# Optimization experiments

Hardware: AMD Instinct MI355X
Metric: run time of the kernel (lower is better)

The kernel has to match this reference:

```python
import jax, jax.numpy as jnp
import numpy as np

D = 1024      # hidden_dim
E = 8         # num_experts
F = 512       # expert_dim


def setup_inputs() -> dict:
    key = jax.random.key(0)
    ks = jax.random.split(key, 7)
    B, N = 4, 4096
    s1 = 1.0 / np.sqrt(D)
    s2 = 1.0 / np.sqrt(F)
    return {
        "x": jax.random.normal(ks[0], (B, N, D), dtype=jnp.float32),
        "W1": jax.random.uniform(ks[1], (E, D, F), jnp.float32, -s1, s1),  # per-expert first linear
        "b1": jax.random.uniform(ks[2], (E, F), jnp.float32, -s1, s1),
        "W2": jax.random.uniform(ks[3], (E, F, D), jnp.float32, -s2, s2),  # per-expert second linear
        "b2": jax.random.uniform(ks[4], (E, D), jnp.float32, -s2, s2),
        "Wr": jax.random.uniform(ks[5], (D, E), jnp.float32, -s1, s1),    # router
        "br": jax.random.uniform(ks[6], (E,), jnp.float32, -s1, s1),
    }


def reference(x, W1, b1, W2, b2, Wr, br):
    # Router: softmax over experts per token. [B,N,E]
    router_weights = jax.nn.softmax(x @ Wr + br, axis=-1)
    # All experts on all tokens (dense soft-MoE), batched as grouped GEMMs.
    h = jax.nn.gelu(jnp.einsum('bnd,edf->bnef', x, W1) + b1, approximate=False)  # [B,N,E,F]
    y = jnp.einsum('bnef,efd->bned', h, W2) + b2[None, None]                      # [B,N,E,D]
    # Softmax-weighted combine over experts.
    return jnp.einsum('bned,bne->bnd', y, router_weights)
```

## Files before the change

### kernel.cpp

```cpp
#include <hip/hip_runtime.h>
#include <hip/hip_bf16.h>
#include <math.h>

#define MTOK 16384
#define DDIM 1024
#define EEXP 8
#define FDIM 512
#define EFK  4096

typedef __attribute__((ext_vector_type(8))) short short8;
typedef __attribute__((ext_vector_type(4))) float floatx4;

__device__ __forceinline__ void gld_lds16(const void* g, void* l) {
  __builtin_amdgcn_global_load_lds((const __attribute__((address_space(1))) void*)g,
                                   (__attribute__((address_space(3))) void*)l, 16, 0, 0);
}

__device__ __forceinline__ float gelu_fast(float v) {
  const float z  = v * 0.70710678118654752f;
  const float az = fabsf(z);
  const float t  = __builtin_amdgcn_rcpf(1.f + 0.3275911f * az);
  const float poly = t * (0.254829592f +
                     t * (-0.284496736f +
                     t * (1.421413741f +
                     t * (-1.453152027f +
                     t * 1.061405429f))));
  const float ex = __expf(-az * az);
  float erfv = 1.f - poly * ex;
  erfv = copysignf(erfv, z);
  return 0.5f * v * (1.f + erfv);
}

__global__ __launch_bounds__(256) void transpose_cast_kernel(
    const float* __restrict__ in, __hip_bfloat16* __restrict__ out, int R, int C) {
  __shared__ float tile[32][33];
  const float* inb = in + (size_t)blockIdx.z * R * C;
  __hip_bfloat16* outb = out + (size_t)blockIdx.z * R * C;
  const int c0 = blockIdx.x * 32, r0 = blockIdx.y * 32;
  const int tx = threadIdx.x & 31, ty = threadIdx.x >> 5;
#pragma unroll
  for (int i = 0; i < 4; ++i)
    tile[ty + i * 8][tx] = inb[(size_t)(r0 + ty + i * 8) * C + (c0 + tx)];
  __syncthreads();
#pragma unroll
  for (int i = 0; i < 4; ++i)
    outb[(size_t)(c0 + ty + i * 8) * R + (r0 + tx)] = __float2bfloat16(tile[tx][ty + i * 8]);
}

__global__ __launch_bounds__(256) void router_cast_kernel(
    const float* __restrict__ x, const float* __restrict__ Wr, const float* __restrict__ br,
    __hip_bfloat16* __restrict__ xbf, float* __restrict__ r) {
  const int wave = (blockIdx.x * 256 + threadIdx.x) >> 6;
  const int lane = threadIdx.x & 63;
  const float* xr = x + (size_t)wave * DDIM;
  float acc[EEXP];
#pragma unroll
  for (int e = 0; e < EEXP; ++e) acc[e] = 0.f;
#pragma unroll
  for (int i = 0; i < DDIM / 64; ++i) {
    const int d = i * 64 + lane;
    const float xv = xr[d];
    xbf[(size_t)wave * DDIM + d] = __float2bfloat16(xv);
    const float4* w4 = (const float4*)(Wr + (size_t)d * EEXP);
    const float4 w0 = w4[0], w1 = w4[1];
    acc[0] += xv * w0.x; acc[1] += xv * w0.y; acc[2] += xv * w0.z; acc[3] += xv * w0.w;
    acc[4] += xv * w1.x; acc[5] += xv * w1.y; acc[6] += xv * w1.z; acc[7] += xv * w1.w;
  }
#pragma unroll
  for (int off = 32; off; off >>= 1) {
#pragma unroll
    for (int e = 0; e < EEXP; ++e) acc[e] += __shfl_xor(acc[e], off, 64);
  }
  float mx = -1e30f;
#pragma unroll
  for (int e = 0; e < EEXP; ++e) { acc[e] += br[e]; mx = fmaxf(mx, acc[e]); }
  float s = 0.f;
#pragma unroll
  for (int e = 0; e < EEXP; ++e) { acc[e] = expf(acc[e] - mx); s += acc[e]; }
  const float inv = 1.f / s;
  if (lane < EEXP) r[(size_t)wave * EEXP + lane] = acc[lane] * inv;
}

#define BUFSZ 65536
#define AOFF  0
#define BOFF  32768

#define STAGE_A(Q1, QM, K0)                                                        \
  do {                                                                             \
    _Pragma("unroll") for (int r_ = 0; r_ < 2; ++r_) {                             \
      gld_lds16(gA + (size_t)(r_ * 128 + (QM) * 64 + wid * 8 + l3) * LDA_ +        \
                    (K0) + ((l7 ^ l3) * 8),                                        \
                ldsb + (Q1) * BUFSZ + AOFF + (QM) * 16384 +                        \
                    (r_ * 64 + wid * 8) * 128);                                    \
    }                                                                              \
  } while (0)

#define STAGE_B(Q1, QN, K0)                                                        \
  do {                                                                             \
    _Pragma("unroll") for (int r_ = 0; r_ < 2; ++r_) {                             \
      const int lin_ = r_ * 64 + wid * 8 + l3;                                     \
      gld_lds16(gB + (size_t)((lin_ >> 5) * 64 + (QN) * 32 + (lin_ & 31)) * LDB_ + \
                    (K0) + ((l7 ^ l3) * 8),                                        \
                ldsb + (Q1) * BUFSZ + BOFF + (QN) * 16384 +                        \
                    (r_ * 64 + wid * 8) * 128);                                    \
    }                                                                              \
  } while (0)

#define STAGE_ALL(Q1, K0)                                                          \
  do { STAGE_A(Q1, 0, K0); STAGE_B(Q1, 0, K0); STAGE_B(Q1, 1, K0);                 \
       STAGE_A(Q1, 1, K0); } while (0)

#define READS_A(P, QM)                                                             \
  _Pragma("unroll") for (int i_ = 0; i_ < 4; ++i_)                                 \
    _Pragma("unroll") for (int k_ = 0; k_ < 2; ++k_)                               \
      af[QM][i_][k_] = *(const short8*)(ldsb + (P) * BUFSZ + AOFF +                \
          (QM) * 16384 + (wr * 64 + i_ * 16 + lanem) * 128 +                       \
          (((k_ * 4 + laneq) ^ swz) * 16));

#define READS_B(P)                                                                 \
  _Pragma("unroll") for (int n_ = 0; n_ < 4; ++n_)                                 \
    _Pragma("unroll") for (int k_ = 0; k_ < 2; ++k_)                               \
      bf[n_][k_] = *(const short8*)(ldsb + (P) * BUFSZ + BOFF +                    \
          (n_ >> 1) * 16384 + (wc * 32 + (n_ & 1) * 16 + lanem) * 128 +            \
          (((k_ * 4 + laneq) ^ swz) * 16));

#define MFMA_Q(QM, QN)                                                             \
  _Pragma("unroll") for (int k_ = 0; k_ < 2; ++k_)                                 \
    _Pragma("unroll") for (int i_ = 0; i_ < 4; ++i_)                               \
      _Pragma("unroll") for (int j_ = 0; j_ < 2; ++j_)                             \
        acc[(QM) * 4 + i_][(QN) * 2 + j_] =                                        \
            __builtin_amdgcn_mfma_f32_16x16x32_bf16(                               \
                af[QM][i_][k_], bf[(QN) * 2 + j_][k_],                             \
                acc[(QM) * 4 + i_][(QN) * 2 + j_], 0, 0, 0);

#define LGKM(N)                                                                    \
  asm volatile("s_waitcnt lgkmcnt(" #N ")" ::: "memory");                          \
  __builtin_amdgcn_sched_barrier(0)

#define GEMM_CORE(NT)                                                              \
  STAGE_ALL(0, 0);                                                                 \
  asm volatile("s_waitcnt vmcnt(0)\n\ts_barrier" ::: "memory");                    \
  for (int kt = 0; kt < (NT); ++kt) {                                              \
    const int p_ = kt & 1;                                                         \
    if (kt + 1 < (NT)) STAGE_ALL(p_ ^ 1, (kt + 1) * 64);                           \
    READS_A(p_, 0);                                                                \
    READS_B(p_);                                                                   \
    __builtin_amdgcn_sched_barrier(0);                                             \
    READS_A(p_, 1);                                                                \
    __builtin_amdgcn_sched_barrier(0);                                             \
    LGKM(12);                                                                      \
    __builtin_amdgcn_s_setprio(1);                                                 \
    MFMA_Q(0, 0);                                                                  \
    __builtin_amdgcn_s_setprio(0);                                                 \
    LGKM(8);                                                                       \
    __builtin_amdgcn_s_setprio(1);                                                 \
    MFMA_Q(0, 1);                                                                  \
    __builtin_amdgcn_s_setprio(0);                                                 \
    LGKM(0);                                                                       \
    __builtin_amdgcn_s_setprio(1);                                                 \
    MFMA_Q(1, 1);                                                                  \
    MFMA_Q(1, 0);                                                                  \
    __builtin_amdgcn_s_setprio(0);                                                 \
    asm volatile("s_waitcnt vmcnt(0)\n\ts_barrier" ::: "memory");                  \
  }

__global__ __launch_bounds__(512, 2) void gemm_h_kernel(
    const __hip_bfloat16* __restrict__ A, const __hip_bfloat16* __restrict__ W1t,
    const float* __restrict__ b1, const float* __restrict__ r,
    __hip_bfloat16* __restrict__ Hs) {
  const int bid = blockIdx.x;
  const int strip = bid & 63, fb = (bid >> 6) & 1, e = bid >> 7;
  const int T0 = strip * 256, F0 = fb * 256;

  __shared__ char ldsb[2 * BUFSZ];

  const int tid = threadIdx.x, lane = tid & 63, wid = tid >> 6;
  const int wr = wid >> 2, wc = wid & 3;
  const int lanem = lane & 15, laneq = lane >> 4;
  const int l3 = lane >> 3, l7 = lane & 7;
  const int swz = lanem & 7;
  const int LDA_ = DDIM, LDB_ = DDIM;

  const __hip_bfloat16* gA = W1t + (size_t)e * FDIM * DDIM + (size_t)F0 * DDIM;
  const __hip_bfloat16* gB = A + (size_t)T0 * DDIM;

  floatx4 acc[8][4];
#pragma unroll
  for (int i = 0; i < 8; ++i)
#pragma unroll
    for (int j = 0; j < 4; ++j) acc[i][j] = (floatx4){0.f, 0.f, 0.f, 0.f};
  short8 af[2][4][2], bf[4][2];

  GEMM_CORE(DDIM / 64);

#pragma unroll
  for (int nj = 0; nj < 4; ++nj) {
    const int tok = T0 + wc * 64 + nj * 16 + lanem;
    const float rv = r[(size_t)tok * EEXP + e];
#pragma unroll
    for (int mi = 0; mi < 8; ++mi) {
      const int f = F0 + wr * 128 + mi * 16 + laneq * 4;
      const float4 b4 = *(const float4*)(b1 + e * FDIM + f);
      union { ushort4 u; __hip_bfloat16 h[4]; } pk;
      pk.h[0] = __float2bfloat16(gelu_fast(acc[mi][nj][0] + b4.x) * rv);
      pk.h[1] = __float2bfloat16(gelu_fast(acc[mi][nj][1] + b4.y) * rv);
      pk.h[2] = __float2bfloat16(gelu_fast(acc[mi][nj][2] + b4.z) * rv);
      pk.h[3] = __float2bfloat16(gelu_fast(acc[mi][nj][3] + b4.w) * rv);
      *(ushort4*)(Hs + (size_t)tok * EFK + e * FDIM + f) = pk.u;
    }
  }
}

__global__ __launch_bounds__(512, 2) void gemm_out_kernel(
    const __hip_bfloat16* __restrict__ Hs, const __hip_bfloat16* __restrict__ W2t,
    const float* __restrict__ b2, const float* __restrict__ r,
    float* __restrict__ out) {
  const int bid = blockIdx.x;
  const int strip = (bid >> 5) * 8 + (bid & 7);
  const int dq = (bid >> 3) & 3;
  const int T0 = strip * 256, D0 = dq * 256;

  __shared__ char ldsb[2 * BUFSZ];

  const int tid = threadIdx.x, lane = tid & 63, wid = tid >> 6;
  const int wr = wid >> 2, wc = wid & 3;
  const int lanem = lane & 15, laneq = lane >> 4;
  const int l3 = lane >> 3, l7 = lane & 7;
  const int swz = lanem & 7;
  const int LDA_ = EFK, LDB_ = EFK;

  const __hip_bfloat16* gA = W2t + (size_t)D0 * EFK;
  const __hip_bfloat16* gB = Hs + (size_t)T0 * EFK;

  floatx4 acc[8][4];
#pragma unroll
  for (int i = 0; i < 8; ++i)
#pragma unroll
    for (int j = 0; j < 4; ++j) acc[i][j] = (floatx4){0.f, 0.f, 0.f, 0.f};
  short8 af[2][4][2], bf[4][2];

  GEMM_CORE(EFK / 64);

#pragma unroll
  for (int mi = 0; mi < 8; ++mi) {
    const int d0 = D0 + wr * 128 + mi * 16 + laneq * 4;
    float4 b2v[EEXP];
#pragma unroll
    for (int e = 0; e < EEXP; ++e) b2v[e] = *(const float4*)(b2 + e * DDIM + d0);
#pragma unroll
    for (int nj = 0; nj < 4; ++nj) {
      const int tok = T0 + wc * 64 + nj * 16 + lanem;
      const float4* r4 = (const float4*)(r + (size_t)tok * EEXP);
      const float4 r0 = r4[0], r1 = r4[1];
      const float rv[EEXP] = {r0.x, r0.y, r0.z, r0.w, r1.x, r1.y, r1.z, r1.w};
      float bx = 0.f, by = 0.f, bz = 0.f, bw = 0.f;
#pragma unroll
      for (int e = 0; e < EEXP; ++e) {
        bx += rv[e] * b2v[e].x; by += rv[e] * b2v[e].y;
        bz += rv[e] * b2v[e].z; bw += rv[e] * b2v[e].w;
      }
      float4 o;
      o.x = acc[mi][nj][0] + bx; o.y = acc[mi][nj][1] + by;
      o.z = acc[mi][nj][2] + bz; o.w = acc[mi][nj][3] + bw;
      *(float4*)(out + (size_t)tok * DDIM + d0) = o;
    }
  }
}

extern "C" void kernel_launch(void* const* d_in, const int* in_sizes, int n_in,
                              void* d_out, int out_size, void* d_ws, size_t ws_size,
                              hipStream_t stream) {
  const float* x  = (const float*)d_in[0];
  const float* W1 = (const float*)d_in[1];
  const float* b1 = (const float*)d_in[2];
  const float* W2 = (const float*)d_in[3];
  const float* b2 = (const float*)d_in[4];
  const float* Wr = (const float*)d_in[5];
  const float* br = (const float*)d_in[6];
  float* out = (float*)d_out;

  char* ws = (char*)d_ws;
  __hip_bfloat16* xbf = (__hip_bfloat16*)(ws);
  __hip_bfloat16* W1t = (__hip_bfloat16*)(ws + (32u << 20));
  __hip_bfloat16* W2t = (__hip_bfloat16*)(ws + (40u << 20));
  float*          r   = (float*)(ws + (48u << 20));
  __hip_bfloat16* Hs  = (__hip_bfloat16*)(ws + (48u << 20) + (1u << 19));

  transpose_cast_kernel<<<dim3(FDIM / 32, DDIM / 32, EEXP), 256, 0, stream>>>(W1, W1t, DDIM, FDIM);
  transpose_cast_kernel<<<dim3(DDIM / 32, EFK / 32, 1), 256, 0, stream>>>(W2, W2t, EFK, DDIM);
  router_cast_kernel<<<MTOK / 4, 256, 0, stream>>>(x, Wr, br, xbf, r);
  gemm_h_kernel<<<dim3((MTOK / 256) * (FDIM / 256) * EEXP), 512, 0, stream>>>(xbf, W1t, b1, r, Hs);
  gemm_out_kernel<<<dim3((MTOK / 256) * (DDIM / 256)), 512, 0, stream>>>(Hs, W2t, b2, r, out);
}
```

Baseline: 470.1 us.

## Interleave quadrant-granular global->LDS staging with MFMA phases in GEMM core

Restructures the double-buffered GEMM main loop into four phases. Each phase reads one A or B quadrant fragment from LDS, issues the global->LDS load for a matching quadrant of a future K-tile, and runs one quarter of the MFMAs. Prefetch now runs up to two tiles ahead with partial vmcnt waits instead of draining all loads each iteration, and the A fragment register array is halved to cut VGPR pressure. The cost is many more s_barrier syncs per iteration and tighter correctness dependencies on buffer reuse timing.

```diff
diff --git a/kernel.cpp b/kernel.cpp
--- a/kernel.cpp
+++ b/kernel.cpp
@@ -106,62 +106,76 @@
     }                                                                              \
   } while (0)
 
-#define STAGE_ALL(Q1, K0)                                                          \
-  do { STAGE_A(Q1, 0, K0); STAGE_B(Q1, 0, K0); STAGE_B(Q1, 1, K0);                 \
-       STAGE_A(Q1, 1, K0); } while (0)
-
-#define READS_A(P, QM)                                                             \
+#define READS_AF(P, QM)                                                            \
   _Pragma("unroll") for (int i_ = 0; i_ < 4; ++i_)                                 \
     _Pragma("unroll") for (int k_ = 0; k_ < 2; ++k_)                               \
-      af[QM][i_][k_] = *(const short8*)(ldsb + (P) * BUFSZ + AOFF +                \
+      af[i_][k_] = *(const short8*)(ldsb + (P) * BUFSZ + AOFF +                    \
           (QM) * 16384 + (wr * 64 + i_ * 16 + lanem) * 128 +                       \
           (((k_ * 4 + laneq) ^ swz) * 16));
 
-#define READS_B(P)                                                                 \
-  _Pragma("unroll") for (int n_ = 0; n_ < 4; ++n_)                                 \
+#define READS_BH(P, QN)                                                            \
+  _Pragma("unroll") for (int j_ = 0; j_ < 2; ++j_)                                 \
     _Pragma("unroll") for (int k_ = 0; k_ < 2; ++k_)                               \
-      bf[n_][k_] = *(const short8*)(ldsb + (P) * BUFSZ + BOFF +                    \
-          (n_ >> 1) * 16384 + (wc * 32 + (n_ & 1) * 16 + lanem) * 128 +            \
+      bf[(QN) * 2 + j_][k_] = *(const short8*)(ldsb + (P) * BUFSZ + BOFF +         \
+          (QN) * 16384 + (wc * 32 + j_ * 16 + lanem) * 128 +                       \
           (((k_ * 4 + laneq) ^ swz) * 16));
 
 #define MFMA_Q(QM, QN)                                                             \
+  __builtin_amdgcn_s_setprio(1);                                                   \
   _Pragma("unroll") for (int k_ = 0; k_ < 2; ++k_)                                 \
     _Pragma("unroll") for (int i_ = 0; i_ < 4; ++i_)                               \
       _Pragma("unroll") for (int j_ = 0; j_ < 2; ++j_)                             \
         acc[(QM) * 4 + i_][(QN) * 2 + j_] =                                        \
             __builtin_amdgcn_mfma_f32_16x16x32_bf16(                               \
-                af[QM][i_][k_], bf[(QN) * 2 + j_][k_],                             \
-                acc[(QM) * 4 + i_][(QN) * 2 + j_], 0, 0, 0);
-
-#define LGKM(N)                                                                    \
-  asm volatile("s_waitcnt lgkmcnt(" #N ")" ::: "memory");                          \
+                af[i_][k_], bf[(QN) * 2 + j_][k_],                                 \
+                acc[(QM) * 4 + i_][(QN) * 2 + j_], 0, 0, 0);                       \
+  __builtin_amdgcn_s_setprio(0);
+
+#define LGKM0                                                                      \
+  asm volatile("s_waitcnt lgkmcnt(0)" ::: "memory");                               \
   __builtin_amdgcn_sched_barrier(0)
 
 #define GEMM_CORE(NT)                                                              \
-  STAGE_ALL(0, 0);                                                                 \
-  asm volatile("s_waitcnt vmcnt(0)\n\ts_barrier" ::: "memory");                    \
+  STAGE_A(0, 0, 0); STAGE_B(0, 0, 0); STAGE_B(0, 1, 0); STAGE_A(0, 1, 0);          \
+  STAGE_A(1, 0, 64); STAGE_B(1, 0, 64); STAGE_B(1, 1, 64);                         \
+  asm volatile("s_waitcnt vmcnt(6)\n\ts_barrier" ::: "memory");                    \
   for (int kt = 0; kt < (NT); ++kt) {                                              \
-    const int p_ = kt & 1;                                                         \
-    if (kt + 1 < (NT)) STAGE_ALL(p_ ^ 1, (kt + 1) * 64);                           \
-    READS_A(p_, 0);                                                                \
-    READS_B(p_);                                                                   \
+    const int p_ = kt & 1, q_ = p_ ^ 1;                                            \
+                                                       \
+    READS_AF(p_, 0);                                                               \
+    READS_BH(p_, 0);                                                               \
+    if (kt + 1 < (NT)) STAGE_A(q_, 1, (kt + 1) * 64);                              \
+    asm volatile("s_waitcnt lgkmcnt(8)" ::: "memory");                             \
     __builtin_amdgcn_sched_barrier(0);                                             \
-    READS_A(p_, 1);                                                                \
-    __builtin_amdgcn_sched_barrier(0);                                             \
-    LGKM(12);                                                                      \
-    __builtin_amdgcn_s_setprio(1);                                                 \
+    __builtin_amdgcn_s_barrier();                                                  \
+    LGKM0;                                                                         \
     MFMA_Q(0, 0);                                                                  \
-    __builtin_amdgcn_s_setprio(0);                                                 \
-    LGKM(8);                                                                       \
-    __builtin_amdgcn_s_setprio(1);                                                 \
+    __builtin_amdgcn_s_barrier();                                                  \
+                                                       \
+    READS_BH(p_, 1);                                                               \
+    if (kt + 2 < (NT)) STAGE_A(p_, 0, (kt + 2) * 64);                              \
+    __builtin_amdgcn_s_barrier();                                                  \
+    LGKM0;                                                                         \
     MFMA_Q(0, 1);                                                                  \
-    __builtin_amdgcn_s_setprio(0);                                                 \
-    LGKM(0);                                                                       \
-    __builtin_amdgcn_s_setprio(1);                                                 \
+    __builtin_amdgcn_s_barrier();                                                  \
+                                                       \
+    READS_AF(p_, 1);                                                               \
+    if (kt + 2 < (NT)) STAGE_B(p_, 1, (kt + 2) * 64);                              \
+    __builtin_amdgcn_s_barrier();                                                  \
+    LGKM0;                                                                         \
     MFMA_Q(1, 1);                                                                  \
+    __builtin_amdgcn_s_barrier();                                                  \
+                                            \
+    if (kt + 2 < (NT)) {                                                           \
+      STAGE_B(p_, 0, (kt + 2) * 64);                                               \
+      asm volatile("s_waitcnt vmcnt(6)\n\ts_barrier" ::: "memory");                \
+    } else if (kt + 1 < (NT)) {                                                    \
+      asm volatile("s_waitcnt vmcnt(0)\n\ts_barrier" ::: "memory");                \
+    } else {                                                                       \
+      __builtin_amdgcn_s_barrier();                                                \
+    }                                                                              \
     MFMA_Q(1, 0);                                                                  \
-    __builtin_amdgcn_s_setprio(0);                                                 \
-    asm volatile("s_waitcnt vmcnt(0)\n\ts_barrier" ::: "memory");                  \
+    __builtin_amdgcn_s_barrier();                                                  \
   }
 
 __global__ __launch_bounds__(512, 2) void gemm_h_kernel(
@@ -189,7 +203,7 @@
   for (int i = 0; i < 8; ++i)
 #pragma unroll
     for (int j = 0; j < 4; ++j) acc[i][j] = (floatx4){0.f, 0.f, 0.f, 0.f};
-  short8 af[2][4][2], bf[4][2];
+  short8 af[4][2], bf[4][2];
 
   GEMM_CORE(DDIM / 64);
 
@@ -237,7 +251,7 @@
   for (int i = 0; i < 8; ++i)
 #pragma unroll
     for (int j = 0; j < 4; ++j) acc[i][j] = (floatx4){0.f, 0.f, 0.f, 0.f};
-  short8 af[2][4][2], bf[4][2];
+  short8 af[4][2], bf[4][2];
 
   GEMM_CORE(EFK / 64);
 
```

New measurement: 478.6 us. Within noise of the previous version (+1.8%).

## Pre-pack weights into MFMA fragment layout and load A directly to registers

Applied to the files above, without the earlier changes.

Replaces the weight transpose-cast kernels with kernels that write W1/W2 as bf16 already laid out in MFMA A-fragment order. The GEMM kernels then load the weight operand straight from global memory into registers, prefetched one k-step ahead, instead of staging it through LDS. This halves LDS use and removes the LDS reads for A. The cost is more global loads in flight and more registers per thread. The pipeline also changes from fine-grained lgkmcnt waits to a vmcnt-based wait that keeps some loads outstanding.

```diff
diff --git a/kernel.cpp b/kernel.cpp
--- a/kernel.cpp
+++ b/kernel.cpp
@@ -31,20 +31,33 @@
   return 0.5f * v * (1.f + erfv);
 }
 
-__global__ __launch_bounds__(256) void transpose_cast_kernel(
-    const float* __restrict__ in, __hip_bfloat16* __restrict__ out, int R, int C) {
-  __shared__ float tile[32][33];
-  const float* inb = in + (size_t)blockIdx.z * R * C;
-  __hip_bfloat16* outb = out + (size_t)blockIdx.z * R * C;
-  const int c0 = blockIdx.x * 32, r0 = blockIdx.y * 32;
-  const int tx = threadIdx.x & 31, ty = threadIdx.x >> 5;
-#pragma unroll
-  for (int i = 0; i < 4; ++i)
-    tile[ty + i * 8][tx] = inb[(size_t)(r0 + ty + i * 8) * C + (c0 + tx)];
-  __syncthreads();
-#pragma unroll
-  for (int i = 0; i < 4; ++i)
-    outb[(size_t)(c0 + ty + i * 8) * R + (r0 + tx)] = __float2bfloat16(tile[tx][ty + i * 8]);
+
+__global__ __launch_bounds__(256) void frag_cast_w2(
+    const float* __restrict__ W2, __hip_bfloat16* __restrict__ W2f) {
+  const int gid  = blockIdx.x * 4 + (threadIdx.x >> 6);
+  const int lane = threadIdx.x & 63;
+  const int kb = gid >> 6, mf = gid & 63;
+  const int d  = mf * 16 + (lane & 15);
+  const int k0 = kb * 32 + (lane >> 4) * 8;
+  union { short8 v; __hip_bfloat16 h[8]; } pk;
+#pragma unroll
+  for (int i = 0; i < 8; ++i)
+    pk.h[i] = __float2bfloat16(W2[(size_t)(k0 + i) * DDIM + d]);
+  *(short8*)((char*)W2f + (size_t)gid * 1024 + lane * 16) = pk.v;
+}
+
+__global__ __launch_bounds__(256) void frag_cast_w1(
+    const float* __restrict__ W1, __hip_bfloat16* __restrict__ W1f) {
+  const int gid  = blockIdx.x * 4 + (threadIdx.x >> 6);
+  const int lane = threadIdx.x & 63;
+  const int e = gid >> 10, kb = (gid >> 5) & 31, mf = gid & 31;
+  const int f  = mf * 16 + (lane & 15);
+  const int d0 = kb * 32 + (lane >> 4) * 8;
+  union { short8 v; __hip_bfloat16 h[8]; } pk;
+#pragma unroll
+  for (int i = 0; i < 8; ++i)
+    pk.h[i] = __float2bfloat16(W1[((size_t)e * DDIM + d0 + i) * FDIM + f]);
+  *(short8*)((char*)W1f + (size_t)gid * 1024 + lane * 16) = pk.v;
 }
 
 __global__ __launch_bounds__(256) void router_cast_kernel(
@@ -81,115 +94,84 @@
   if (lane < EEXP) r[(size_t)wave * EEXP + lane] = acc[lane] * inv;
 }
 
-#define BUFSZ 65536
-#define AOFF  0
-#define BOFF  32768
-
-#define STAGE_A(Q1, QM, K0)                                                        \
-  do {                                                                             \
-    _Pragma("unroll") for (int r_ = 0; r_ < 2; ++r_) {                             \
-      gld_lds16(gA + (size_t)(r_ * 128 + (QM) * 64 + wid * 8 + l3) * LDA_ +        \
-                    (K0) + ((l7 ^ l3) * 8),                                        \
-                ldsb + (Q1) * BUFSZ + AOFF + (QM) * 16384 +                        \
-                    (r_ * 64 + wid * 8) * 128);                                    \
-    }                                                                              \
-  } while (0)
-
-#define STAGE_B(Q1, QN, K0)                                                        \
+#define BUF_B 32768
+
+#define STAGE_BQ(Q1, QN, K0)                                                       \
   do {                                                                             \
     _Pragma("unroll") for (int r_ = 0; r_ < 2; ++r_) {                             \
       const int lin_ = r_ * 64 + wid * 8 + l3;                                     \
       gld_lds16(gB + (size_t)((lin_ >> 5) * 64 + (QN) * 32 + (lin_ & 31)) * LDB_ + \
                     (K0) + ((l7 ^ l3) * 8),                                        \
-                ldsb + (Q1) * BUFSZ + BOFF + (QN) * 16384 +                        \
+                ldsb + (Q1) * BUF_B + (QN) * 16384 +                               \
                     (r_ * 64 + wid * 8) * 128);                                    \
     }                                                                              \
   } while (0)
 
-#define STAGE_ALL(Q1, K0)                                                          \
-  do { STAGE_A(Q1, 0, K0); STAGE_B(Q1, 0, K0); STAGE_B(Q1, 1, K0);                 \
-       STAGE_A(Q1, 1, K0); } while (0)
-
-#define READS_A(P, QM)                                                             \
-  _Pragma("unroll") for (int i_ = 0; i_ < 4; ++i_)                                 \
-    _Pragma("unroll") for (int k_ = 0; k_ < 2; ++k_)                               \
-      af[QM][i_][k_] = *(const short8*)(ldsb + (P) * BUFSZ + AOFF +                \
-          (QM) * 16384 + (wr * 64 + i_ * 16 + lanem) * 128 +                       \
-          (((k_ * 4 + laneq) ^ swz) * 16));
-
 #define READS_B(P)                                                                 \
   _Pragma("unroll") for (int n_ = 0; n_ < 4; ++n_)                                 \
     _Pragma("unroll") for (int k_ = 0; k_ < 2; ++k_)                               \
-      bf[n_][k_] = *(const short8*)(ldsb + (P) * BUFSZ + BOFF +                    \
+      bf[n_][k_] = *(const short8*)(ldsb + (P) * BUF_B +                           \
           (n_ >> 1) * 16384 + (wc * 32 + (n_ & 1) * 16 + lanem) * 128 +            \
           (((k_ * 4 + laneq) ^ swz) * 16));
 
-#define MFMA_Q(QM, QN)                                                             \
-  _Pragma("unroll") for (int k_ = 0; k_ < 2; ++k_)                                 \
-    _Pragma("unroll") for (int i_ = 0; i_ < 4; ++i_)                               \
-      _Pragma("unroll") for (int j_ = 0; j_ < 2; ++j_)                             \
-        acc[(QM) * 4 + i_][(QN) * 2 + j_] =                                        \
-            __builtin_amdgcn_mfma_f32_16x16x32_bf16(                               \
-                af[QM][i_][k_], bf[(QN) * 2 + j_][k_],                             \
-                acc[(QM) * 4 + i_][(QN) * 2 + j_], 0, 0, 0);
-
-#define LGKM(N)                                                                    \
-  asm volatile("s_waitcnt lgkmcnt(" #N ")" ::: "memory");                          \
-  __builtin_amdgcn_sched_barrier(0)
+#define LOAD_A8(DST, KB)                                                           \
+  _Pragma("unroll") for (int mf_ = 0; mf_ < 8; ++mf_)                              \
+    DST[mf_] = *(const short8*)(gAf + (size_t)(KB) * AKBSTRIDE + mf_ * 1024);
+
+#define MFMA32(AFR, KK)                                                            \
+  __builtin_amdgcn_s_setprio(1);                                                   \
+  _Pragma("unroll") for (int m_ = 0; m_ < 8; ++m_)                                 \
+    _Pragma("unroll") for (int n_ = 0; n_ < 4; ++n_)                               \
+      acc[m_][n_] = __builtin_amdgcn_mfma_f32_16x16x32_bf16(                       \
+          AFR[m_], bf[n_][KK], acc[m_][n_], 0, 0, 0);                              \
+  __builtin_amdgcn_s_setprio(0);
 
 #define GEMM_CORE(NT)                                                              \
-  STAGE_ALL(0, 0);                                                                 \
-  asm volatile("s_waitcnt vmcnt(0)\n\ts_barrier" ::: "memory");                    \
+                              \
+  STAGE_BQ(0, 0, 0); STAGE_BQ(0, 1, 0);                                            \
+  __builtin_amdgcn_sched_barrier(0);                                               \
+  LOAD_A8(afk0, 0); LOAD_A8(afk1, 1);                                              \
   for (int kt = 0; kt < (NT); ++kt) {                                              \
-    const int p_ = kt & 1;                                                         \
-    if (kt + 1 < (NT)) STAGE_ALL(p_ ^ 1, (kt + 1) * 64);                           \
-    READS_A(p_, 0);                                                                \
+    const int p_ = kt & 1, q_ = p_ ^ 1;                                            \
+    asm volatile("s_waitcnt vmcnt(16)\n\ts_barrier" ::: "memory");                 \
+    if (kt + 1 < (NT)) { STAGE_BQ(q_, 0, (kt + 1) * 64);                           \
+                         STAGE_BQ(q_, 1, (kt + 1) * 64); }                         \
+    __builtin_amdgcn_sched_barrier(0);                                             \
     READS_B(p_);                                                                   \
-    __builtin_amdgcn_sched_barrier(0);                                             \
-    READS_A(p_, 1);                                                                \
-    __builtin_amdgcn_sched_barrier(0);                                             \
-    LGKM(12);                                                                      \
-    __builtin_amdgcn_s_setprio(1);                                                 \
-    MFMA_Q(0, 0);                                                                  \
-    __builtin_amdgcn_s_setprio(0);                                                 \
-    LGKM(8);                                                                       \
-    __builtin_amdgcn_s_setprio(1);                                                 \
-    MFMA_Q(0, 1);                                                                  \
-    __builtin_amdgcn_s_setprio(0);                                                 \
-    LGKM(0);                                                                       \
-    __builtin_amdgcn_s_setprio(1);                                                 \
-    MFMA_Q(1, 1);                                                                  \
-    MFMA_Q(1, 0);                                                                  \
-    __builtin_amdgcn_s_setprio(0);                                                 \
-    asm volatile("s_waitcnt vmcnt(0)\n\ts_barrier" ::: "memory");                  \
+    MFMA32(afk0, 0);                                                               \
+    if (kt + 1 < (NT)) LOAD_A8(afk0, 2 * (kt + 1));                                \
+    MFMA32(afk1, 1);                                                               \
+    if (kt + 1 < (NT)) LOAD_A8(afk1, 2 * (kt + 1) + 1);                            \
   }
 
 __global__ __launch_bounds__(512, 2) void gemm_h_kernel(
-    const __hip_bfloat16* __restrict__ A, const __hip_bfloat16* __restrict__ W1t,
+    const __hip_bfloat16* __restrict__ A, const __hip_bfloat16* __restrict__ W1f,
     const float* __restrict__ b1, const float* __restrict__ r,
     __hip_bfloat16* __restrict__ Hs) {
   const int bid = blockIdx.x;
   const int strip = bid & 63, fb = (bid >> 6) & 1, e = bid >> 7;
   const int T0 = strip * 256, F0 = fb * 256;
 
-  __shared__ char ldsb[2 * BUFSZ];
+  __shared__ char ldsb[2 * BUF_B];
 
   const int tid = threadIdx.x, lane = tid & 63, wid = tid >> 6;
   const int wr = wid >> 2, wc = wid & 3;
   const int lanem = lane & 15, laneq = lane >> 4;
   const int l3 = lane >> 3, l7 = lane & 7;
   const int swz = lanem & 7;
-  const int LDA_ = DDIM, LDB_ = DDIM;
-
-  const __hip_bfloat16* gA = W1t + (size_t)e * FDIM * DDIM + (size_t)F0 * DDIM;
+  const int LDB_ = DDIM;
+  const size_t AKBSTRIDE = 32 * 1024;
+
   const __hip_bfloat16* gB = A + (size_t)T0 * DDIM;
+  const char* gAf = (const char*)W1f + ((size_t)e * 1024 +
+                    (F0 >> 4) + wr * 8) * 1024 + (size_t)lane * 16;
 
   floatx4 acc[8][4];
 #pragma unroll
   for (int i = 0; i < 8; ++i)
 #pragma unroll
     for (int j = 0; j < 4; ++j) acc[i][j] = (floatx4){0.f, 0.f, 0.f, 0.f};
-  short8 af[2][4][2], bf[4][2];
+  short8 afk0[8], afk1[8], bf[4][2];
 
   GEMM_CORE(DDIM / 64);
 
@@ -212,7 +194,7 @@
 }
 
 __global__ __launch_bounds__(512, 2) void gemm_out_kernel(
-    const __hip_bfloat16* __restrict__ Hs, const __hip_bfloat16* __restrict__ W2t,
+    const __hip_bfloat16* __restrict__ Hs, const __hip_bfloat16* __restrict__ W2f,
     const float* __restrict__ b2, const float* __restrict__ r,
     float* __restrict__ out) {
   const int bid = blockIdx.x;
@@ -220,24 +202,26 @@
   const int dq = (bid >> 3) & 3;
   const int T0 = strip * 256, D0 = dq * 256;
 
-  __shared__ char ldsb[2 * BUFSZ];
+  __shared__ char ldsb[2 * BUF_B];
 
   const int tid = threadIdx.x, lane = tid & 63, wid = tid >> 6;
   const int wr = wid >> 2, wc = wid & 3;
   const int lanem = lane & 15, laneq = lane >> 4;
   const int l3 = lane >> 3, l7 = lane & 7;
   const int swz = lanem & 7;
-  const int LDA_ = EFK, LDB_ = EFK;
-
-  const __hip_bfloat16* gA = W2t + (size_t)D0 * EFK;
+  const int LDB_ = EFK;
+  const size_t AKBSTRIDE = 64 * 1024;
+
   const __hip_bfloat16* gB = Hs + (size_t)T0 * EFK;
+  const char* gAf = (const char*)W2f + ((size_t)(D0 >> 4) + wr * 8) * 1024 +
+                    (size_t)lane * 16;
 
   floatx4 acc[8][4];
 #pragma unroll
   for (int i = 0; i < 8; ++i)
 #pragma unroll
     for (int j = 0; j < 4; ++j) acc[i][j] = (floatx4){0.f, 0.f, 0.f, 0.f};
-  short8 af[2][4][2], bf[4][2];
+  short8 afk0[8], afk1[8], bf[4][2];
 
   GEMM_CORE(EFK / 64);
 
@@ -281,14 +265,14 @@
 
   char* ws = (char*)d_ws;
   __hip_bfloat16* xbf = (__hip_bfloat16*)(ws);
-  __hip_bfloat16* W1t = (__hip_bfloat16*)(ws + (32u << 20));
-  __hip_bfloat16* W2t = (__hip_bfloat16*)(ws + (40u << 20));
+  __hip_bfloat16* W1f = (__hip_bfloat16*)(ws + (32u << 20));
+  __hip_bfloat16* W2f = (__hip_bfloat16*)(ws + (40u << 20));
   float*          r   = (float*)(ws + (48u << 20));
   __hip_bfloat16* Hs  = (__hip_bfloat16*)(ws + (48u << 20) + (1u << 19));
 
-  transpose_cast_kernel<<<dim3(FDIM / 32, DDIM / 32, EEXP), 256, 0, stream>>>(W1, W1t, DDIM, FDIM);
-  transpose_cast_kernel<<<dim3(DDIM / 32, EFK / 32, 1), 256, 0, stream>>>(W2, W2t, EFK, DDIM);
+  frag_cast_w1<<<2048, 256, 0, stream>>>(W1, W1f);
+  frag_cast_w2<<<2048, 256, 0, stream>>>(W2, W2f);
   router_cast_kernel<<<MTOK / 4, 256, 0, stream>>>(x, Wr, br, xbf, r);
-  gemm_h_kernel<<<dim3((MTOK / 256) * (FDIM / 256) * EEXP), 512, 0, stream>>>(xbf, W1t, b1, r, Hs);
-  gemm_out_kernel<<<dim3((MTOK / 256) * (DDIM / 256)), 512, 0, stream>>>(Hs, W2t, b2, r, out);
-}
+  gemm_h_kernel<<<dim3((MTOK / 256) * (FDIM / 256) * EEXP), 512, 0, stream>>>(xbf, W1f, b1, r, Hs);
+  gemm_out_kernel<<<dim3((MTOK / 256) * (DDIM / 256)), 512, 0, stream>>>(Hs, W2f, b2, r, out);
+}
```

Result: slower. 516.1 us (+9.8%).
